# Kernel tuning notes

Measured on AMD Instinct MI355X. Metric: run time of the kernel, lower is better.

## Reference

```python
import jax, jax.numpy as jnp
import numpy as np

H, C = 8, 32          # heads, channels per head; H*C = 256 triggers the LN branch
N_NODES = 30000       # nodes per node type
N_EDGES = 100000      # edges per edge type
N_TYPES = 6           # hardwired edge types (all src = Package_Name)
D_IN = 128            # raw input feature dim (Package_Name stays at 128)
LRELU_SLOPE = 0.2     # PyG GATConv default negative_slope


def _segment_softmax(e, dst, n):
    # softmax of per-edge logits e [E,H] grouped by destination node
    m = jax.ops.segment_max(e, dst, num_segments=n)
    ex = jnp.exp(e - m[dst])
    den = jax.ops.segment_sum(ex, dst, num_segments=n)
    return ex / (den[dst] + 1e-16)


def _gat(x_src, x_tgt, src, dst, Ws, Wd, a_s, a_d, b):
    # bipartite GATConv, concat heads, no self loops, no edge features
    hs = (x_src @ Ws).reshape(-1, H, C)   # [Ns,H,C]
    hd = (x_tgt @ Wd).reshape(-1, H, C)   # [Nt,H,C]
    es = jnp.einsum('nhc,hc->nh', hs, a_s)
    ed = jnp.einsum('nhc,hc->nh', hd, a_d)
    e = jax.nn.leaky_relu(es[src] + ed[dst], negative_slope=LRELU_SLOPE)  # [E,H]
    n = x_tgt.shape[0]
    alpha = _segment_softmax(e, dst, n)                                   # [E,H]
    msg = hs[src] * alpha[:, :, None]                                     # [E,H,C]
    out = jax.ops.segment_sum(msg, dst, num_segments=n).reshape(n, H * C) + b
    return out, alpha


def _ln_relu(x, g, b):
    mu = x.mean(-1, keepdims=True)
    var = ((x - mu) ** 2).mean(-1, keepdims=True)
    return jax.nn.relu((x - mu) / jnp.sqrt(var + 1e-5) * g + b)


def setup_inputs() -> dict:
    key = jax.random.key(0)
    ks = jax.random.split(key, 16)
    s = 0.05
    return {
        'x_pkg': jax.random.normal(ks[0], (N_NODES, D_IN), jnp.float32),
        'x_tgt': jax.random.normal(ks[1], (N_TYPES, N_NODES, D_IN), jnp.float32),
        'edge_index': jax.random.randint(ks[2], (N_TYPES, 2, N_EDGES), 0, N_NODES, jnp.int32),
        'W1_src': jax.random.normal(ks[3], (N_TYPES, D_IN, H * C), jnp.float32) * s,
        'W1_dst': jax.random.normal(ks[4], (N_TYPES, D_IN, H * C), jnp.float32) * s,
        'att1_src': jax.random.normal(ks[5], (N_TYPES, H, C), jnp.float32) * s,
        'att1_dst': jax.random.normal(ks[6], (N_TYPES, H, C), jnp.float32) * s,
        'b1': jnp.zeros((N_TYPES, H * C), jnp.float32),
        'W2_src': jax.random.normal(ks[7], (N_TYPES, D_IN, H * C), jnp.float32) * s,
        'W2_dst': jax.random.normal(ks[8], (N_TYPES, H * C, H * C), jnp.float32) * s,
        'att2_src': jax.random.normal(ks[9], (N_TYPES, H, C), jnp.float32) * s,
        'att2_dst': jax.random.normal(ks[10], (N_TYPES, H, C), jnp.float32) * s,
        'b2': jnp.zeros((N_TYPES, H * C), jnp.float32),
        'gamma': jnp.ones((N_TYPES, H * C), jnp.float32),
        'beta': jnp.zeros((N_TYPES, H * C), jnp.float32),
        'Wc': jax.random.normal(ks[11], (N_TYPES * H * C + D_IN, 1), jnp.float32) * s,
        'bc': jnp.zeros((1,), jnp.float32),
    }


def reference(x_pkg, x_tgt, edge_index, W1_src, W1_dst, att1_src, att1_dst, b1,
              W2_src, W2_dst, att2_src, att2_dst, b2, gamma, beta, Wc, bc):
    def layer(xt, ei, Ws, Wd, a_s, a_d, bb):
        return _gat(x_pkg, xt, ei[0], ei[1], Ws, Wd, a_s, a_d, bb)

    vlayer = jax.vmap(layer, in_axes=(0, 0, 0, 0, 0, 0, 0))

    # layer 1: Package_Name -> each of 6 target types; Package_Name itself unchanged
    out1, _ = vlayer(x_tgt, edge_index, W1_src, W1_dst, att1_src, att1_dst, b1)
    x1 = jax.vmap(_ln_relu)(out1, gamma, beta)   # module reuses ln1 after both layers

    # layer 2: src features are still the raw 128-d Package_Name features
    out2, alpha2 = vlayer(x1, edge_index, W2_src, W2_dst, att2_src, att2_dst, b2)
    x2 = jax.vmap(_ln_relu)(out2, gamma, beta)

    # global mean pool per node type, concat (6 targets then Package_Name), classify
    pooled = jnp.concatenate([x2.mean(axis=1).reshape(-1), x_pkg.mean(axis=0)])
    logits = pooled @ Wc[:, 0] + bc[0]
    return logits, alpha2
```

## Files before the change

kernel.cpp:

```cpp
#include <hip/hip_runtime.h>
#include <hip/hip_bf16.h>
#include <cstddef>

#define N_NODES 30000
#define N_EDGES 100000
#define N_TYPES 6
#define D_IN 128
#define HC 256
#define NH 8
#define CH 32

typedef __attribute__((ext_vector_type(8))) unsigned short ushort8_t;
typedef __attribute__((ext_vector_type(4))) unsigned short ushort4_t;
typedef __attribute__((ext_vector_type(8))) __bf16 bf16x8;
typedef __attribute__((ext_vector_type(4))) float floatx4;

#define FG_GRID (N_NODES / 4)

__device__ inline unsigned short f2bf(float f) {
    unsigned u = __float_as_uint(f);
    u += 0x7fffu + ((u >> 16) & 1u);
    return (unsigned short)(u >> 16);
}
__device__ inline float bf2f(unsigned short u) {
    return __uint_as_float(((unsigned)u) << 16);
}

__global__ void zero4(float4* __restrict__ p, int n4) {
    int g = blockIdx.x * blockDim.x + threadIdx.x;
    if (g < n4) p[g] = make_float4(0.f, 0.f, 0.f, 0.f);
}
__global__ void zero_i(int* __restrict__ p, int n) {
    int g = blockIdx.x * blockDim.x + threadIdx.x;
    if (g < n) p[g] = 0;
}
__global__ void to_bf16(const float* __restrict__ x, unsigned short* __restrict__ o, int n4) {
    int g = blockIdx.x * blockDim.x + threadIdx.x;
    if (g >= n4) return;
    float4 v = ((const float4*)x)[g];
    ushort4_t p;
    p[0] = f2bf(v.x); p[1] = f2bf(v.y); p[2] = f2bf(v.z); p[3] = f2bf(v.w);
    *(ushort4_t*)&o[(size_t)g * 4] = p;
}

__global__ void hist_all(const int* __restrict__ ei, int* __restrict__ counts) {
    int t = blockIdx.y;
    int e = blockIdx.x * 256 + threadIdx.x;
    if (e < N_EDGES)
        atomicAdd(&counts[t * N_NODES + ei[(size_t)t * 2 * N_EDGES + N_EDGES + e]], 1);
}

#define SCAN_T 1024
#define SCAN_C 30
__global__ __launch_bounds__(1024) void scan_all(const int* __restrict__ counts_g,
                                                 int* __restrict__ row_ptr_g,
                                                 int* __restrict__ cursor_g) {
    int t = blockIdx.x;
    const int* counts = counts_g + t * N_NODES;
    int* row_ptr = row_ptr_g + t * (N_NODES + 1);
    int* cursor = cursor_g + t * N_NODES;
    __shared__ int part[SCAN_T];
    int tid = threadIdx.x;
    int base = tid * SCAN_C;
    int loc[SCAN_C];
    int s = 0;
    #pragma unroll
    for (int i = 0; i < SCAN_C; ++i) {
        int idx = base + i;
        int v = (idx < N_NODES) ? counts[idx] : 0;
        loc[i] = s; s += v;
    }
    part[tid] = s;
    __syncthreads();
    int tot = s;
    for (int d = 1; d < SCAN_T; d <<= 1) {
        int v = (tid >= d) ? part[tid - d] : 0;
        __syncthreads();
        part[tid] += v;
        __syncthreads();
    }
    int off = part[tid] - tot;
    #pragma unroll
    for (int i = 0; i < SCAN_C; ++i) {
        int idx = base + i;
        if (idx < N_NODES) { int r = off + loc[i]; row_ptr[idx] = r; cursor[idx] = r; }
    }
    if (tid == SCAN_T - 1) row_ptr[N_NODES] = part[SCAN_T - 1];
}

__global__ void fill_all(const int* __restrict__ ei, const int* __restrict__ row_ptr_g,
                         int* __restrict__ cursor,
                         int* __restrict__ elist, int* __restrict__ edense) {
    int t = blockIdx.y;
    int e = blockIdx.x * 256 + threadIdx.x;
    if (e < N_EDGES) {
        const int* src = ei + (size_t)t * 2 * N_EDGES;
        const int* dst = src + N_EDGES;
        const int d = dst[e];
        int pos = atomicAdd(&cursor[t * N_NODES + d], 1);
        elist[t * N_EDGES + pos] = src[e];
        int loc = pos - row_ptr_g[t * (N_NODES + 1) + d];
        if (loc < 4)
            edense[((size_t)t * N_NODES + d) * 4 + loc] = src[e];
    }
}

__global__ void att_weight_all(const float* __restrict__ W1d, const float* __restrict__ a1d,
                               const float* __restrict__ W2d, const float* __restrict__ a2d,
                               float* __restrict__ wd1, float* __restrict__ wd2) {
    int g = blockIdx.x * blockDim.x + threadIdx.x;
    const int per_t = (D_IN + HC) * NH;
    if (g >= N_TYPES * per_t) return;
    int t = g / per_t, r = g % per_t;
    if (r < D_IN * NH) {
        int k = r >> 3, h = r & 7;
        const float* wr = W1d + (size_t)t * D_IN * HC + (size_t)k * HC + h * CH;
        const float* ar = a1d + t * HC + h * CH;
        float s = 0.f;
        #pragma unroll
        for (int c = 0; c < CH; ++c) s += wr[c] * ar[c];
        wd1[t * D_IN * NH + h * D_IN + k] = s;
    } else {
        r -= D_IN * NH;
        int k = r >> 3, h = r & 7;
        const float* wr = W2d + (size_t)t * HC * HC + (size_t)k * HC + h * CH;
        const float* ar = a2d + t * HC + h * CH;
        float s = 0.f;
        #pragma unroll
        for (int c = 0; c < CH; ++c) s += wr[c] * ar[c];
        wd2[t * HC * NH + h * HC + k] = s;
    }
}

__global__ __launch_bounds__(256) void wt_prep(const float* __restrict__ W1s,
                                               const float* __restrict__ W2s,
                                               unsigned short* __restrict__ Wt) {
    const int j = blockIdx.z;
    const float* W = (j < 6) ? W1s + (size_t)j * D_IN * HC
                             : W2s + (size_t)(j - 6) * D_IN * HC;
    const int n0 = blockIdx.x * 64;
    const int k0 = blockIdx.y * 32;
    __shared__ unsigned short tile[32][71];
    const int t = threadIdx.x;
    {
        const int k = t >> 3, n = (t & 7) * 8;
        const float4 a = *(const float4*)&W[(size_t)(k0 + k) * HC + n0 + n];
        const float4 b = *(const float4*)&W[(size_t)(k0 + k) * HC + n0 + n + 4];
        tile[k][n + 0] = f2bf(a.x); tile[k][n + 1] = f2bf(a.y);
        tile[k][n + 2] = f2bf(a.z); tile[k][n + 3] = f2bf(a.w);
        tile[k][n + 4] = f2bf(b.x); tile[k][n + 5] = f2bf(b.y);
        tile[k][n + 6] = f2bf(b.z); tile[k][n + 7] = f2bf(b.w);
    }
    __syncthreads();
    {
        const int n = t >> 2, k = (t & 3) * 8;
        ushort8_t v;
        #pragma unroll
        for (int q = 0; q < 8; ++q) v[q] = tile[k + q][n];
        *(ushort8_t*)&Wt[((size_t)j * HC + n0 + n) * D_IN + k0 + k] = v;
    }
}

__global__ __launch_bounds__(256) void ed1_all(const float* __restrict__ x_tgt,
                                               const float* __restrict__ wd1,
                                               float* __restrict__ ed1g) {
    const int t = blockIdx.y;
    const int lane = threadIdx.x & 63;
    const int wv = threadIdx.x >> 6;
    const int n8 = lane >> 3, h = lane & 7;
    const int node = blockIdx.x * 32 + wv * 8 + n8;
    if (node >= N_NODES) return;
    const float* xr = x_tgt + ((size_t)t * N_NODES + node) * D_IN;
    const float* wp = wd1 + t * D_IN * NH + h * D_IN;
    float acc = 0.f;
    #pragma unroll
    for (int k = 0; k < D_IN; k += 4) {
        const float4 x4 = *(const float4*)&xr[k];
        const float4 w4 = *(const float4*)&wp[k];
        acc += x4.x * w4.x + x4.y * w4.y + x4.z * w4.z + x4.w * w4.w;
    }
    ed1g[((size_t)t * N_NODES + node) * NH + h] = acc;
}

__global__ __launch_bounds__(256) void gemm_all(const unsigned short* __restrict__ A,
                                                const unsigned short* __restrict__ Wt,
                                                const float* __restrict__ att1,
                                                const float* __restrict__ att2,
                                                unsigned short* __restrict__ hs_all,
                                                float* __restrict__ es_all) {
    const int j = blockIdx.z;
    const unsigned short* B = Wt + (size_t)j * HC * D_IN;
    const float* att = (j < 6) ? att1 + j * HC : att2 + (j - 6) * HC;
    unsigned short* Cp = hs_all + (size_t)j * N_NODES * HC;
    float* e_out = es_all + (size_t)j * N_NODES * NH;

    __shared__ __align__(16) unsigned short As[64 * 136];
    __shared__ __align__(16) unsigned short Bs[128 * 136];

    const int tid = threadIdx.x;
    const int w = tid >> 6;
    const int lane = tid & 63;
    const int col = lane & 15;
    const int quad = lane >> 4;
    const int m0 = blockIdx.x * 64;
    const int n0 = blockIdx.y * 128;

    {
        const int r = tid >> 2;
        const int kc = (tid & 3) * 8;
        const int gm = m0 + r;
        #pragma unroll
        for (int c = 0; c < 4; ++c) {
            ushort8_t v = (ushort8_t){0, 0, 0, 0, 0, 0, 0, 0};
            if (gm < N_NODES) v = *(const ushort8_t*)&A[(size_t)gm * D_IN + kc + c * 32];
            *(ushort8_t*)&As[r * 136 + kc + c * 32] = v;
        }
    }
    {
        const int r = tid >> 1;
        const int ks = (tid & 1) * 64;
        const unsigned short* br = &B[(size_t)(n0 + r) * D_IN + ks];
        #pragma unroll
        for (int q = 0; q < 8; ++q) {
            ushort8_t v = *(const ushort8_t*)&br[q * 8];
            *(ushort8_t*)&Bs[r * 136 + ks + q * 8] = v;
        }
    }
    __syncthreads();

    floatx4 acc[8];
    #pragma unroll
    for (int ct = 0; ct < 8; ++ct) acc[ct] = (floatx4){0.f, 0.f, 0.f, 0.f};

    #pragma unroll
    for (int ks = 0; ks < 4; ++ks) {
        ushort8_t araw = *(const ushort8_t*)&As[(w * 16 + col) * 136 + ks * 32 + quad * 8];
        bf16x8 af = __builtin_bit_cast(bf16x8, araw);
        #pragma unroll
        for (int ct = 0; ct < 8; ++ct) {
            ushort8_t braw = *(const ushort8_t*)&Bs[(ct * 16 + col) * 136 + ks * 32 + quad * 8];
            bf16x8 bf = __builtin_bit_cast(bf16x8, braw);
            acc[ct] = __builtin_amdgcn_mfma_f32_16x16x32_bf16(af, bf, acc[ct], 0, 0, 0);
        }
    }

    float attv[8];
    #pragma unroll
    for (int ct = 0; ct < 8; ++ct) attv[ct] = att[n0 + ct * 16 + col];
    const int hbase = n0 >> 5;
    #pragma unroll
    for (int r = 0; r < 4; ++r) {
        float h0v = acc[0][r] * attv[0] + acc[1][r] * attv[1];
        float h1v = acc[2][r] * attv[2] + acc[3][r] * attv[3];
        float h2v = acc[4][r] * attv[4] + acc[5][r] * attv[5];
        float h3v = acc[6][r] * attv[6] + acc[7][r] * attv[7];
        #pragma unroll
        for (int off = 1; off < 16; off <<= 1) {
            h0v += __shfl_xor(h0v, off);
            h1v += __shfl_xor(h1v, off);
            h2v += __shfl_xor(h2v, off);
            h3v += __shfl_xor(h3v, off);
        }
        if (col == 0) {
            int gm = m0 + w * 16 + quad * 4 + r;
            if (gm < N_NODES)
                *(float4*)&e_out[gm * NH + hbase] = make_float4(h0v, h1v, h2v, h3v);
        }
    }

    __syncthreads();
    unsigned short* Cs = (unsigned short*)Bs;
    #pragma unroll
    for (int ct = 0; ct < 8; ++ct) {
        const int cc = ct * 16 + col;
        #pragma unroll
        for (int r = 0; r < 4; ++r)
            Cs[(w * 16 + quad * 4 + r) * 144 + cc] = f2bf(acc[ct][r]);
    }
    __syncthreads();
    {
        const int r = tid >> 2;
        const int c0 = (tid & 3) * 32;
        const int gm = m0 + r;
        if (gm < N_NODES) {
            #pragma unroll
            for (int q = 0; q < 4; ++q) {
                ushort8_t v = *(const ushort8_t*)&Cs[r * 144 + c0 + q * 8];
                *(ushort8_t*)&Cp[(size_t)gm * HC + n0 + c0 + q * 8] = v;
            }
        }
    }
}

__device__ inline void edge4(const float* __restrict__ es,
                             const unsigned short* __restrict__ hs,
                             int s_pre, int i, int cm,
                             int h_l, int lane, float ed_mine,
                             float& den, float4& acc) {
    const int i1 = (i + 1 < cm) ? i + 1 : cm;
    const int i2 = (i + 2 < cm) ? i + 2 : cm;
    const int i3 = (i + 3 < cm) ? i + 3 : cm;
    const int s0 = __shfl(s_pre, i);
    const int s1 = __shfl(s_pre, i1);
    const int s2 = __shfl(s_pre, i2);
    const int s3 = __shfl(s_pre, i3);
    float q0 = es[s0 * NH + h_l];
    float q1 = es[s1 * NH + h_l];
    float q2 = es[s2 * NH + h_l];
    float q3 = es[s3 * NH + h_l];
    const ushort4_t v0 = *(const ushort4_t*)&hs[(size_t)s0 * HC + lane * 4];
    const ushort4_t v1 = *(const ushort4_t*)&hs[(size_t)s1 * HC + lane * 4];
    const ushort4_t v2 = *(const ushort4_t*)&hs[(size_t)s2 * HC + lane * 4];
    const ushort4_t v3 = *(const ushort4_t*)&hs[(size_t)s3 * HC + lane * 4];
    q0 += ed_mine; q0 = (q0 >= 0.f) ? q0 : 0.2f * q0;
    q1 += ed_mine; q1 = (q1 >= 0.f) ? q1 : 0.2f * q1;
    q2 += ed_mine; q2 = (q2 >= 0.f) ? q2 : 0.2f * q2;
    q3 += ed_mine; q3 = (q3 >= 0.f) ? q3 : 0.2f * q3;
    const float x0 = __expf(q0);
    const float x1 = (i + 1 <= cm) ? __expf(q1) : 0.f;
    const float x2 = (i + 2 <= cm) ? __expf(q2) : 0.f;
    const float x3 = (i + 3 <= cm) ? __expf(q3) : 0.f;
    den += (x0 + x1) + (x2 + x3);
    acc.x += x0 * bf2f(v0[0]) + x1 * bf2f(v1[0]) + x2 * bf2f(v2[0]) + x3 * bf2f(v3[0]);
    acc.y += x0 * bf2f(v0[1]) + x1 * bf2f(v1[1]) + x2 * bf2f(v2[1]) + x3 * bf2f(v3[1]);
    acc.z += x0 * bf2f(v0[2]) + x1 * bf2f(v1[2]) + x2 * bf2f(v2[2]) + x3 * bf2f(v3[2]);
    acc.w += x0 * bf2f(v0[3]) + x1 * bf2f(v1[3]) + x2 * bf2f(v2[3]) + x3 * bf2f(v3[3]);
}

__device__ inline void edge1(const float* __restrict__ es,
                             const unsigned short* __restrict__ hs,
                             int s, int h_l, int lane, float ed_mine,
                             float& den, float4& acc) {
    float x = es[s * NH + h_l] + ed_mine;
    x = (x >= 0.f) ? x : 0.2f * x;
    const float ex = __expf(x);
    den += ex;
    const ushort4_t hv = *(const ushort4_t*)&hs[(size_t)s * HC + lane * 4];
    acc.x += ex * bf2f(hv[0]); acc.y += ex * bf2f(hv[1]);
    acc.z += ex * bf2f(hv[2]); acc.w += ex * bf2f(hv[3]);
}

__global__ __launch_bounds__(256) void fused_gather_all(
        const int* __restrict__ row_ptr_g, const int* __restrict__ elist_g,
        const int* __restrict__ edense_g,
        const float* __restrict__ es_all, const float* __restrict__ ed1g,
        const unsigned short* __restrict__ hs_all,
        const float* __restrict__ b1, const float* __restrict__ b2,
        const float* __restrict__ gamma, const float* __restrict__ beta,
        const float* __restrict__ wd2,
        float* __restrict__ ed2g_all, float* __restrict__ deng_all,
        float* __restrict__ ppart) {
    const int t = blockIdx.y;
    const int* row_ptr = row_ptr_g + t * (N_NODES + 1);
    const int* elist = elist_g + t * N_EDGES;
    const int* eden = edense_g + (size_t)t * N_NODES * 4;
    const float* es1 = es_all + (size_t)t * N_NODES * NH;
    const float* es2 = es_all + (size_t)(6 + t) * N_NODES * NH;
    const unsigned short* hs1 = hs_all + (size_t)t * N_NODES * HC;
    const unsigned short* hs2 = hs_all + (size_t)(6 + t) * N_NODES * HC;
    const float* gam = gamma + t * HC;
    const float* bet = beta + t * HC;
    const float* w2 = wd2 + t * HC * NH;
    float* ed2g = ed2g_all + (size_t)t * N_NODES * NH;
    float* deng = deng_all + (size_t)t * N_NODES * NH;

    const int lane = threadIdx.x & 63;
    const int w = threadIdx.x >> 6;
    const int d = blockIdx.x * 4 + w;
    const int h_l = lane >> 3;

    const float ed_mine = ed1g[((size_t)t * N_NODES + d) * NH + h_l];
    int dw = 0;
    if (lane < 4) dw = eden[d * 4 + lane];
    const int e0 = row_ptr[d], e1n = row_ptr[d + 1];
    const int cnt = e1n - e0;
    const bool fast = (cnt > 0) && (cnt <= 4);

    int s_pre = 0;
    if (!fast) {
        if (lane < cnt) s_pre = elist[e0 + lane];
    }

    float den1 = 0.f, den2 = 0.f;
    float4 acc1 = make_float4(0.f, 0.f, 0.f, 0.f);
    float4 acc2 = make_float4(0.f, 0.f, 0.f, 0.f);

    float q20, q21, q22, q23;
    ushort4_t v20, v21, v22, v23;

    if (fast) {
        const int s0 = __shfl(dw, 0);
        const int s1 = __shfl(dw, 1);
        const int s2 = __shfl(dw, 2);
        const int s3 = __shfl(dw, 3);
        float q10 = es1[s0 * NH + h_l];
        float q11 = es1[s1 * NH + h_l];
        float q12 = es1[s2 * NH + h_l];
        float q13 = es1[s3 * NH + h_l];
        const ushort4_t v10 = *(const ushort4_t*)&hs1[(size_t)s0 * HC + lane * 4];
        const ushort4_t v11 = *(const ushort4_t*)&hs1[(size_t)s1 * HC + lane * 4];
        const ushort4_t v12 = *(const ushort4_t*)&hs1[(size_t)s2 * HC + lane * 4];
        const ushort4_t v13 = *(const ushort4_t*)&hs1[(size_t)s3 * HC + lane * 4];
        q20 = es2[s0 * NH + h_l];
        q21 = es2[s1 * NH + h_l];
        q22 = es2[s2 * NH + h_l];
        q23 = es2[s3 * NH + h_l];
        v20 = *(const ushort4_t*)&hs2[(size_t)s0 * HC + lane * 4];
        v21 = *(const ushort4_t*)&hs2[(size_t)s1 * HC + lane * 4];
        v22 = *(const ushort4_t*)&hs2[(size_t)s2 * HC + lane * 4];
        v23 = *(const ushort4_t*)&hs2[(size_t)s3 * HC + lane * 4];
        q10 += ed_mine; q10 = (q10 >= 0.f) ? q10 : 0.2f * q10;
        q11 += ed_mine; q11 = (q11 >= 0.f) ? q11 : 0.2f * q11;
        q12 += ed_mine; q12 = (q12 >= 0.f) ? q12 : 0.2f * q12;
        q13 += ed_mine; q13 = (q13 >= 0.f) ? q13 : 0.2f * q13;
        const float x0 = __expf(q10);
        const float x1 = (cnt > 1) ? __expf(q11) : 0.f;
        const float x2 = (cnt > 2) ? __expf(q12) : 0.f;
        const float x3 = (cnt > 3) ? __expf(q13) : 0.f;
        den1 = (x0 + x1) + (x2 + x3);
        acc1.x = x0 * bf2f(v10[0]) + x1 * bf2f(v11[0]) + x2 * bf2f(v12[0]) + x3 * bf2f(v13[0]);
        acc1.y = x0 * bf2f(v10[1]) + x1 * bf2f(v11[1]) + x2 * bf2f(v12[1]) + x3 * bf2f(v13[1]);
        acc1.z = x0 * bf2f(v10[2]) + x1 * bf2f(v11[2]) + x2 * bf2f(v12[2]) + x3 * bf2f(v13[2]);
        acc1.w = x0 * bf2f(v10[3]) + x1 * bf2f(v11[3]) + x2 * bf2f(v12[3]) + x3 * bf2f(v13[3]);
    } else if (cnt > 0) {
        const int c1 = (cnt < 64) ? cnt : 64;
        const int cm = c1 - 1;
        for (int i = 0; i < c1; i += 4)
            edge4(es1, hs1, s_pre, i, cm, h_l, lane, ed_mine, den1, acc1);
        if (cnt > 64)
            for (int ii = e0 + 64; ii < e1n; ++ii)
                edge1(es1, hs1, elist[ii], h_l, lane, ed_mine, den1, acc1);
    }

    const float inv1 = 1.f / (den1 + 1e-16f);
    const float4 bv1 = *(const float4*)&b1[t * HC + lane * 4];
    acc1.x = acc1.x * inv1 + bv1.x; acc1.y = acc1.y * inv1 + bv1.y;
    acc1.z = acc1.z * inv1 + bv1.z; acc1.w = acc1.w * inv1 + bv1.w;

    float s1 = acc1.x + acc1.y + acc1.z + acc1.w;
    float s2 = acc1.x * acc1.x + acc1.y * acc1.y + acc1.z * acc1.z + acc1.w * acc1.w;
    #pragma unroll
    for (int off = 1; off < 64; off <<= 1) { s1 += __shfl_xor(s1, off); s2 += __shfl_xor(s2, off); }
    const float mu = s1 * (1.f / 256.f);
    const float var = s2 * (1.f / 256.f) - mu * mu;
    const float rstd = rsqrtf(var + 1e-5f);
    const float4 g4 = *(const float4*)&gam[lane * 4];
    const float4 b4 = *(const float4*)&bet[lane * 4];
    const float ya0 = fmaxf((acc1.x - mu) * rstd * g4.x + b4.x, 0.f);
    const float ya1 = fmaxf((acc1.y - mu) * rstd * g4.y + b4.y, 0.f);
    const float ya2 = fmaxf((acc1.z - mu) * rstd * g4.z + b4.z, 0.f);
    const float ya3 = fmaxf((acc1.w - mu) * rstd * g4.w + b4.w, 0.f);

    __shared__ __align__(16) float ya_s[4][256];
    {
        const int c0 = lane * 4;
        const int widx = (c0 & ~31) | ((c0 & 31) ^ ((lane >> 3) << 2));
        *(float4*)&ya_s[w][widx] = make_float4(ya0, ya1, ya2, ya3);
    }
    const int k8 = lane >> 3;
    const int hh = lane & 7;
    const float* w2h = w2 + hh * HC;
    float e2 = 0.f;
    #pragma unroll
    for (int jj = 0; jj < 8; ++jj) {
        const int idx = k8 * 32 + ((jj * 4) ^ (k8 << 2));
        const float4 y = *(const float4*)&ya_s[w][idx];
        const float4 wv = *(const float4*)&w2h[k8 * 32 + jj * 4];
        e2 += y.x * wv.x + y.y * wv.y + y.z * wv.z + y.w * wv.w;
    }
    e2 += __shfl_xor(e2, 8);
    e2 += __shfl_xor(e2, 16);
    e2 += __shfl_xor(e2, 32);
    if (lane < 8) ed2g[d * NH + lane] = e2;
    const float ed2_mine = __shfl(e2, h_l);

    if (fast) {
        q20 += ed2_mine; q20 = (q20 >= 0.f) ? q20 : 0.2f * q20;
        q21 += ed2_mine; q21 = (q21 >= 0.f) ? q21 : 0.2f * q21;
        q22 += ed2_mine; q22 = (q22 >= 0.f) ? q22 : 0.2f * q22;
        q23 += ed2_mine; q23 = (q23 >= 0.f) ? q23 : 0.2f * q23;
        const float x0 = __expf(q20);
        const float x1 = (cnt > 1) ? __expf(q21) : 0.f;
        const float x2 = (cnt > 2) ? __expf(q22) : 0.f;
        const float x3 = (cnt > 3) ? __expf(q23) : 0.f;
        den2 = (x0 + x1) + (x2 + x3);
        acc2.x = x0 * bf2f(v20[0]) + x1 * bf2f(v21[0]) + x2 * bf2f(v22[0]) + x3 * bf2f(v23[0]);
        acc2.y = x0 * bf2f(v20[1]) + x1 * bf2f(v21[1]) + x2 * bf2f(v22[1]) + x3 * bf2f(v23[1]);
        acc2.z = x0 * bf2f(v20[2]) + x1 * bf2f(v21[2]) + x2 * bf2f(v22[2]) + x3 * bf2f(v23[2]);
        acc2.w = x0 * bf2f(v20[3]) + x1 * bf2f(v21[3]) + x2 * bf2f(v22[3]) + x3 * bf2f(v23[3]);
    } else if (cnt > 0) {
        const int c1 = (cnt < 64) ? cnt : 64;
        const int cm = c1 - 1;
        for (int i = 0; i < c1; i += 4)
            edge4(es2, hs2, s_pre, i, cm, h_l, lane, ed2_mine, den2, acc2);
        if (cnt > 64)
            for (int ii = e0 + 64; ii < e1n; ++ii)
                edge1(es2, hs2, elist[ii], h_l, lane, ed2_mine, den2, acc2);
    }

    if ((lane & 7) == 0) deng[d * NH + h_l] = den2;
    const float inv2 = 1.f / (den2 + 1e-16f);
    const float4 bv2 = *(const float4*)&b2[t * HC + lane * 4];
    acc2.x = acc2.x * inv2 + bv2.x; acc2.y = acc2.y * inv2 + bv2.y;
    acc2.z = acc2.z * inv2 + bv2.z; acc2.w = acc2.w * inv2 + bv2.w;

    float t1 = acc2.x + acc2.y + acc2.z + acc2.w;
    float t2 = acc2.x * acc2.x + acc2.y * acc2.y + acc2.z * acc2.z + acc2.w * acc2.w;
    #pragma unroll
    for (int off = 1; off < 64; off <<= 1) { t1 += __shfl_xor(t1, off); t2 += __shfl_xor(t2, off); }
    const float mu2 = t1 * (1.f / 256.f);
    const float var2 = t2 * (1.f / 256.f) - mu2 * mu2;
    const float rstd2 = rsqrtf(var2 + 1e-5f);
    float4 pool;
    pool.x = fmaxf((acc2.x - mu2) * rstd2 * g4.x + b4.x, 0.f);
    pool.y = fmaxf((acc2.y - mu2) * rstd2 * g4.y + b4.y, 0.f);
    pool.z = fmaxf((acc2.z - mu2) * rstd2 * g4.z + b4.z, 0.f);
    pool.w = fmaxf((acc2.w - mu2) * rstd2 * g4.w + b4.w, 0.f);

    __shared__ __align__(16) float sacc[4][260];
    *(float4*)&sacc[w][lane * 4] = pool;
    __syncthreads();
    const int tid = threadIdx.x;
    float tot = sacc[0][tid] + sacc[1][tid] + sacc[2][tid] + sacc[3][tid];
    ppart[((size_t)t * FG_GRID + blockIdx.x) * HC + tid] = tot;
}

__global__ __launch_bounds__(256) void pool_reduce_all(const float* __restrict__ ppart,
                                                       float* __restrict__ psums) {
    int t = blockIdx.y;
    const float* part = ppart + (size_t)t * FG_GRID * HC;
    int tid = threadIdx.x;
    float acc = 0.f;
    for (int b = blockIdx.x; b < FG_GRID; b += gridDim.x)
        acc += part[(size_t)b * HC + tid];
    atomicAdd(&psums[t * HC + tid], acc);
}

__global__ __launch_bounds__(256) void alpha_all(const int* __restrict__ ei,
                          const float* __restrict__ es_all,
                          const float* __restrict__ ed2g_all,
                          const float* __restrict__ deng_all,
                          float* __restrict__ out) {
    int t = blockIdx.y;
    int e = blockIdx.x * 256 + threadIdx.x;
    if (e >= N_EDGES) return;
    const int* src = ei + (size_t)t * 2 * N_EDGES;
    const int* dst = src + N_EDGES;
    const int s = src[e], d = dst[e];
    const float* esp = es_all + (size_t)(6 + t) * N_NODES * NH + (size_t)s * NH;
    const float* edp = ed2g_all + (size_t)t * N_NODES * NH + (size_t)d * NH;
    const float* dnp = deng_all + (size_t)t * N_NODES * NH + (size_t)d * NH;
    const float4 ea = *(const float4*)esp;
    const float4 eb = *(const float4*)(esp + 4);
    const float4 da = *(const float4*)edp;
    const float4 db = *(const float4*)(edp + 4);
    const float4 na = *(const float4*)dnp;
    const float4 nb = *(const float4*)(dnp + 4);
    float x[8];
    x[0] = ea.x + da.x; x[1] = ea.y + da.y; x[2] = ea.z + da.z; x[3] = ea.w + da.w;
    x[4] = eb.x + db.x; x[5] = eb.y + db.y; x[6] = eb.z + db.z; x[7] = eb.w + db.w;
    float n[8] = {na.x, na.y, na.z, na.w, nb.x, nb.y, nb.z, nb.w};
    float* op = out + (size_t)t * N_EDGES * NH + (size_t)e * NH;
    #pragma unroll
    for (int h = 0; h < 8; ++h) {
        float v = x[h];
        v = (v >= 0.f) ? v : 0.2f * v;
        op[h] = __expf(v) / (n[h] + 1e-16f);
    }
}

__global__ __launch_bounds__(256) void pkg_accum(const float* __restrict__ x, float* __restrict__ sums) {
    int tid = threadIdx.x;
    int col = tid & 127;
    int rof = tid >> 7;
    float acc = 0.f;
    for (int r = blockIdx.x * 2 + rof; r < N_NODES; r += gridDim.x * 2)
        acc += x[(size_t)r * D_IN + col];
    atomicAdd(&sums[col], acc);
}

__global__ __launch_bounds__(256) void logits_k(const float* __restrict__ psums,
                                                const float* __restrict__ ksums,
                                                const float* __restrict__ Wc,
                                                const float* __restrict__ bc,
                                                float* __restrict__ out) {
    int tid = threadIdx.x;
    const float inv = 1.f / (float)N_NODES;
    float acc = 0.f;
    for (int i = tid; i < N_TYPES * HC; i += 256) acc += psums[i] * inv * Wc[i];
    if (tid < D_IN) acc += ksums[tid] * inv * Wc[N_TYPES * HC + tid];
    #pragma unroll
    for (int off = 32; off; off >>= 1) acc += __shfl_down(acc, off);
    __shared__ float w[4];
    if ((tid & 63) == 0) w[tid >> 6] = acc;
    __syncthreads();
    if (tid == 0) out[0] = w[0] + w[1] + w[2] + w[3] + bc[0];
}

static inline void zf(float* p, int n, hipStream_t stream) {
    int n4 = (n + 3) >> 2;
    zero4<<<(n4 + 255) / 256, 256, 0, stream>>>((float4*)p, n4);
}

extern "C" void kernel_launch(void* const* d_in, const int* in_sizes, int n_in,
                              void* d_out, int out_size, void* d_ws, size_t ws_size,
                              hipStream_t stream) {
    const float* x_pkg    = (const float*)d_in[0];
    const float* x_tgt    = (const float*)d_in[1];
    const int*   ei       = (const int*)d_in[2];
    const float* W1_src   = (const float*)d_in[3];
    const float* W1_dst   = (const float*)d_in[4];
    const float* att1_src = (const float*)d_in[5];
    const float* att1_dst = (const float*)d_in[6];
    const float* b1       = (const float*)d_in[7];
    const float* W2_src   = (const float*)d_in[8];
    const float* W2_dst   = (const float*)d_in[9];
    const float* att2_src = (const float*)d_in[10];
    const float* att2_dst = (const float*)d_in[11];
    const float* b2       = (const float*)d_in[12];
    const float* gamma    = (const float*)d_in[13];
    const float* beta     = (const float*)d_in[14];
    const float* Wc       = (const float*)d_in[15];
    const float* bc       = (const float*)d_in[16];
    float* out = (float*)d_out;

    char* wsb = (char*)d_ws;
    unsigned short* xpkg_bf = (unsigned short*)wsb;
    unsigned short* hs_all  = xpkg_bf + (size_t)N_NODES * D_IN;
    float* es_all   = (float*)(hs_all + (size_t)12 * N_NODES * HC);
    float* ed2g_all = es_all + (size_t)12 * N_NODES * NH;
    float* deng_all = ed2g_all + (size_t)N_TYPES * N_NODES * NH;
    float* psums    = deng_all + (size_t)N_TYPES * N_NODES * NH;
    float* ksums    = psums + N_TYPES * HC;
    float* wd1      = ksums + D_IN;
    float* wd2      = wd1 + N_TYPES * D_IN * NH;
    unsigned short* Wt = (unsigned short*)(wd2 + N_TYPES * HC * NH);
    float* ed1g     = (float*)(Wt + (size_t)12 * HC * D_IN);
    float* ppart    = ed1g + (size_t)N_TYPES * N_NODES * NH;
    int* counts  = (int*)(ppart + (size_t)N_TYPES * FG_GRID * HC);
    int* row_ptr = counts + N_TYPES * N_NODES;
    int* cursor  = row_ptr + N_TYPES * (N_NODES + 1);
    int* elist   = cursor + N_TYPES * N_NODES;
    int* edense  = elist + N_TYPES * N_EDGES;

    dim3 egrid((N_EDGES + 255) / 256, N_TYPES);

    zf(psums, N_TYPES * HC + D_IN, stream);
    pkg_accum<<<256, 256, 0, stream>>>(x_pkg, ksums);
    {
        int tot = N_TYPES * (D_IN + HC) * NH;
        att_weight_all<<<(tot + 255) / 256, 256, 0, stream>>>(W1_dst, att1_dst, W2_dst, att2_dst, wd1, wd2);
    }
    {
        dim3 g(4, 4, 12);
        wt_prep<<<g, 256, 0, stream>>>(W1_src, W2_src, Wt);
    }
    {
        dim3 g((N_NODES + 31) / 32, N_TYPES);
        ed1_all<<<g, 256, 0, stream>>>(x_tgt, wd1, ed1g);
    }
    to_bf16<<<((N_NODES * D_IN / 4) + 255) / 256, 256, 0, stream>>>(x_pkg, xpkg_bf, N_NODES * D_IN / 4);
    zero_i<<<(N_TYPES * N_NODES + 255) / 256, 256, 0, stream>>>(counts, N_TYPES * N_NODES);
    zero_i<<<(N_TYPES * N_NODES * 4 + 255) / 256, 256, 0, stream>>>(edense, N_TYPES * N_NODES * 4);
    hist_all<<<egrid, 256, 0, stream>>>(ei, counts);
    scan_all<<<N_TYPES, SCAN_T, 0, stream>>>(counts, row_ptr, cursor);
    fill_all<<<egrid, 256, 0, stream>>>(ei, row_ptr, cursor, elist, edense);

    {
        dim3 g((N_NODES + 63) / 64, 2, 12);
        gemm_all<<<g, 256, 0, stream>>>(xpkg_bf, Wt, att1_src, att2_src,
                                        hs_all, es_all);
    }

    {
        dim3 g(FG_GRID, N_TYPES);
        fused_gather_all<<<g, 256, 0, stream>>>(row_ptr, elist, edense, es_all, ed1g, hs_all,
                                                b1, b2, gamma, beta, wd2,
                                                ed2g_all, deng_all, ppart);
    }
    {
        dim3 g(64, N_TYPES);
        pool_reduce_all<<<g, 256, 0, stream>>>(ppart, psums);
    }
    {
        dim3 g((N_EDGES + 255) / 256, N_TYPES);
        alpha_all<<<g, 256, 0, stream>>>(ei, es_all, ed2g_all, deng_all, out + 1);
    }

    logits_k<<<1, 256, 0, stream>>>(psums, ksums, Wc, bc, out);
}
```

Baseline: 848.5 us.

## Process two destination nodes per wavefront with batched fast-path gathers

Each wavefront in the fused gather kernel now handles two destination nodes instead of one, halving the grid. Both nodes' fast-path gathers (attention logits and bf16 features for both layers) are issued up front, so more memory loads are in flight per wave and per-type constants are loaded once. The cost is higher register pressure from holding two FastBuf sets, which may lower occupancy. The shared ya buffer is reused by both nodes in sequence within the same wave.

Measured after the change: 794.2 us. 1.07x faster.

```diff
diff --git a/kernel.cpp b/kernel.cpp
--- a/kernel.cpp
+++ b/kernel.cpp
@@ -15,7 +15,7 @@
 typedef __attribute__((ext_vector_type(8))) __bf16 bf16x8;
 typedef __attribute__((ext_vector_type(4))) float floatx4;
 
-#define FG_GRID (N_NODES / 4)
+#define FG_GRID (N_NODES / 8)
 
 __device__ inline unsigned short f2bf(float f) {
     unsigned u = __float_as_uint(f);
@@ -340,6 +340,156 @@
     acc.z += ex * bf2f(hv[2]); acc.w += ex * bf2f(hv[3]);
 }
 
+struct FastBuf {
+    float q10, q11, q12, q13, q20, q21, q22, q23;
+    ushort4_t v10, v11, v12, v13, v20, v21, v22, v23;
+};
+
+__device__ inline FastBuf node_load_fast(int dw, int h_l, int lane,
+        const float* __restrict__ es1, const float* __restrict__ es2,
+        const unsigned short* __restrict__ hs1, const unsigned short* __restrict__ hs2) {
+    FastBuf b;
+    const int s0 = __shfl(dw, 0);
+    const int s1 = __shfl(dw, 1);
+    const int s2 = __shfl(dw, 2);
+    const int s3 = __shfl(dw, 3);
+    b.q10 = es1[s0 * NH + h_l];
+    b.q11 = es1[s1 * NH + h_l];
+    b.q12 = es1[s2 * NH + h_l];
+    b.q13 = es1[s3 * NH + h_l];
+    b.v10 = *(const ushort4_t*)&hs1[(size_t)s0 * HC + lane * 4];
+    b.v11 = *(const ushort4_t*)&hs1[(size_t)s1 * HC + lane * 4];
+    b.v12 = *(const ushort4_t*)&hs1[(size_t)s2 * HC + lane * 4];
+    b.v13 = *(const ushort4_t*)&hs1[(size_t)s3 * HC + lane * 4];
+    b.q20 = es2[s0 * NH + h_l];
+    b.q21 = es2[s1 * NH + h_l];
+    b.q22 = es2[s2 * NH + h_l];
+    b.q23 = es2[s3 * NH + h_l];
+    b.v20 = *(const ushort4_t*)&hs2[(size_t)s0 * HC + lane * 4];
+    b.v21 = *(const ushort4_t*)&hs2[(size_t)s1 * HC + lane * 4];
+    b.v22 = *(const ushort4_t*)&hs2[(size_t)s2 * HC + lane * 4];
+    b.v23 = *(const ushort4_t*)&hs2[(size_t)s3 * HC + lane * 4];
+    return b;
+}
+
+__device__ inline float4 node_math(
+        bool fast, int cnt, int e0, int e1n, int s_pre, float ed_mine,
+        const FastBuf& fb,
+        const float* __restrict__ es1, const float* __restrict__ es2,
+        const unsigned short* __restrict__ hs1, const unsigned short* __restrict__ hs2,
+        const int* __restrict__ elist,
+        const float4& bv1, const float4& bv2, const float4& g4, const float4& b4,
+        float* ya_row, const float* __restrict__ w2h,
+        int lane, int h_l, int d,
+        float* __restrict__ ed2g, float* __restrict__ deng) {
+    float den1 = 0.f, den2 = 0.f;
+    float4 acc1 = make_float4(0.f, 0.f, 0.f, 0.f);
+    float4 acc2 = make_float4(0.f, 0.f, 0.f, 0.f);
+
+    if (fast) {
+        float q10 = fb.q10 + ed_mine; q10 = (q10 >= 0.f) ? q10 : 0.2f * q10;
+        float q11 = fb.q11 + ed_mine; q11 = (q11 >= 0.f) ? q11 : 0.2f * q11;
+        float q12 = fb.q12 + ed_mine; q12 = (q12 >= 0.f) ? q12 : 0.2f * q12;
+        float q13 = fb.q13 + ed_mine; q13 = (q13 >= 0.f) ? q13 : 0.2f * q13;
+        const float x0 = __expf(q10);
+        const float x1 = (cnt > 1) ? __expf(q11) : 0.f;
+        const float x2 = (cnt > 2) ? __expf(q12) : 0.f;
+        const float x3 = (cnt > 3) ? __expf(q13) : 0.f;
+        den1 = (x0 + x1) + (x2 + x3);
+        acc1.x = x0 * bf2f(fb.v10[0]) + x1 * bf2f(fb.v11[0]) + x2 * bf2f(fb.v12[0]) + x3 * bf2f(fb.v13[0]);
+        acc1.y = x0 * bf2f(fb.v10[1]) + x1 * bf2f(fb.v11[1]) + x2 * bf2f(fb.v12[1]) + x3 * bf2f(fb.v13[1]);
+        acc1.z = x0 * bf2f(fb.v10[2]) + x1 * bf2f(fb.v11[2]) + x2 * bf2f(fb.v12[2]) + x3 * bf2f(fb.v13[2]);
+        acc1.w = x0 * bf2f(fb.v10[3]) + x1 * bf2f(fb.v11[3]) + x2 * bf2f(fb.v12[3]) + x3 * bf2f(fb.v13[3]);
+    } else if (cnt > 0) {
+        const int c1 = (cnt < 64) ? cnt : 64;
+        const int cm = c1 - 1;
+        for (int i = 0; i < c1; i += 4)
+            edge4(es1, hs1, s_pre, i, cm, h_l, lane, ed_mine, den1, acc1);
+        if (cnt > 64)
+            for (int ii = e0 + 64; ii < e1n; ++ii)
+                edge1(es1, hs1, elist[ii], h_l, lane, ed_mine, den1, acc1);
+    }
+
+    const float inv1 = 1.f / (den1 + 1e-16f);
+    acc1.x = acc1.x * inv1 + bv1.x; acc1.y = acc1.y * inv1 + bv1.y;
+    acc1.z = acc1.z * inv1 + bv1.z; acc1.w = acc1.w * inv1 + bv1.w;
+
+    float s1 = acc1.x + acc1.y + acc1.z + acc1.w;
+    float s2 = acc1.x * acc1.x + acc1.y * acc1.y + acc1.z * acc1.z + acc1.w * acc1.w;
+    #pragma unroll
+    for (int off = 1; off < 64; off <<= 1) { s1 += __shfl_xor(s1, off); s2 += __shfl_xor(s2, off); }
+    const float mu = s1 * (1.f / 256.f);
+    const float var = s2 * (1.f / 256.f) - mu * mu;
+    const float rstd = rsqrtf(var + 1e-5f);
+    const float ya0 = fmaxf((acc1.x - mu) * rstd * g4.x + b4.x, 0.f);
+    const float ya1 = fmaxf((acc1.y - mu) * rstd * g4.y + b4.y, 0.f);
+    const float ya2 = fmaxf((acc1.z - mu) * rstd * g4.z + b4.z, 0.f);
+    const float ya3 = fmaxf((acc1.w - mu) * rstd * g4.w + b4.w, 0.f);
+
+    {
+        const int c0 = lane * 4;
+        const int widx = (c0 & ~31) | ((c0 & 31) ^ ((lane >> 3) << 2));
+        *(float4*)&ya_row[widx] = make_float4(ya0, ya1, ya2, ya3);
+    }
+    const int k8 = lane >> 3;
+    float e2 = 0.f;
+    #pragma unroll
+    for (int jj = 0; jj < 8; ++jj) {
+        const int idx = k8 * 32 + ((jj * 4) ^ (k8 << 2));
+        const float4 y = *(const float4*)&ya_row[idx];
+        const float4 wv = *(const float4*)&w2h[k8 * 32 + jj * 4];
+        e2 += y.x * wv.x + y.y * wv.y + y.z * wv.z + y.w * wv.w;
+    }
+    e2 += __shfl_xor(e2, 8);
+    e2 += __shfl_xor(e2, 16);
+    e2 += __shfl_xor(e2, 32);
+    if (lane < 8) ed2g[d * NH + lane] = e2;
+    const float ed2_mine = __shfl(e2, h_l);
+
+    if (fast) {
+        float q20 = fb.q20 + ed2_mine; q20 = (q20 >= 0.f) ? q20 : 0.2f * q20;
+        float q21 = fb.q21 + ed2_mine; q21 = (q21 >= 0.f) ? q21 : 0.2f * q21;
+        float q22 = fb.q22 + ed2_mine; q22 = (q22 >= 0.f) ? q22 : 0.2f * q22;
+        float q23 = fb.q23 + ed2_mine; q23 = (q23 >= 0.f) ? q23 : 0.2f * q23;
+        const float x0 = __expf(q20);
+        const float x1 = (cnt > 1) ? __expf(q21) : 0.f;
+        const float x2 = (cnt > 2) ? __expf(q22) : 0.f;
+        const float x3 = (cnt > 3) ? __expf(q23) : 0.f;
+        den2 = (x0 + x1) + (x2 + x3);
+        acc2.x = x0 * bf2f(fb.v20[0]) + x1 * bf2f(fb.v21[0]) + x2 * bf2f(fb.v22[0]) + x3 * bf2f(fb.v23[0]);
+        acc2.y = x0 * bf2f(fb.v20[1]) + x1 * bf2f(fb.v21[1]) + x2 * bf2f(fb.v22[1]) + x3 * bf2f(fb.v23[1]);
+        acc2.z = x0 * bf2f(fb.v20[2]) + x1 * bf2f(fb.v21[2]) + x2 * bf2f(fb.v22[2]) + x3 * bf2f(fb.v23[2]);
+        acc2.w = x0 * bf2f(fb.v20[3]) + x1 * bf2f(fb.v21[3]) + x2 * bf2f(fb.v22[3]) + x3 * bf2f(fb.v23[3]);
+    } else if (cnt > 0) {
+        const int c1 = (cnt < 64) ? cnt : 64;
+        const int cm = c1 - 1;
+        for (int i = 0; i < c1; i += 4)
+            edge4(es2, hs2, s_pre, i, cm, h_l, lane, ed2_mine, den2, acc2);
+        if (cnt > 64)
+            for (int ii = e0 + 64; ii < e1n; ++ii)
+                edge1(es2, hs2, elist[ii], h_l, lane, ed2_mine, den2, acc2);
+    }
+
+    if ((lane & 7) == 0) deng[d * NH + h_l] = den2;
+    const float inv2 = 1.f / (den2 + 1e-16f);
+    acc2.x = acc2.x * inv2 + bv2.x; acc2.y = acc2.y * inv2 + bv2.y;
+    acc2.z = acc2.z * inv2 + bv2.z; acc2.w = acc2.w * inv2 + bv2.w;
+
+    float t1 = acc2.x + acc2.y + acc2.z + acc2.w;
+    float t2 = acc2.x * acc2.x + acc2.y * acc2.y + acc2.z * acc2.z + acc2.w * acc2.w;
+    #pragma unroll
+    for (int off = 1; off < 64; off <<= 1) { t1 += __shfl_xor(t1, off); t2 += __shfl_xor(t2, off); }
+    const float mu2 = t1 * (1.f / 256.f);
+    const float var2 = t2 * (1.f / 256.f) - mu2 * mu2;
+    const float rstd2 = rsqrtf(var2 + 1e-5f);
+    float4 pool;
+    pool.x = fmaxf((acc2.x - mu2) * rstd2 * g4.x + b4.x, 0.f);
+    pool.y = fmaxf((acc2.y - mu2) * rstd2 * g4.y + b4.y, 0.f);
+    pool.z = fmaxf((acc2.z - mu2) * rstd2 * g4.z + b4.z, 0.f);
+    pool.w = fmaxf((acc2.w - mu2) * rstd2 * g4.w + b4.w, 0.f);
+    return pool;
+}
+
 __global__ __launch_bounds__(256) void fused_gather_all(
         const int* __restrict__ row_ptr_g, const int* __restrict__ elist_g,
         const int* __restrict__ edense_g,
@@ -358,164 +508,58 @@
     const float* es2 = es_all + (size_t)(6 + t) * N_NODES * NH;
     const unsigned short* hs1 = hs_all + (size_t)t * N_NODES * HC;
     const unsigned short* hs2 = hs_all + (size_t)(6 + t) * N_NODES * HC;
-    const float* gam = gamma + t * HC;
-    const float* bet = beta + t * HC;
-    const float* w2 = wd2 + t * HC * NH;
     float* ed2g = ed2g_all + (size_t)t * N_NODES * NH;
     float* deng = deng_all + (size_t)t * N_NODES * NH;
 
     const int lane = threadIdx.x & 63;
     const int w = threadIdx.x >> 6;
-    const int d = blockIdx.x * 4 + w;
+    const int dA = blockIdx.x * 8 + w * 2;
+    const int dB = dA + 1;
     const int h_l = lane >> 3;
 
-    const float ed_mine = ed1g[((size_t)t * N_NODES + d) * NH + h_l];
-    int dw = 0;
-    if (lane < 4) dw = eden[d * 4 + lane];
-    const int e0 = row_ptr[d], e1n = row_ptr[d + 1];
-    const int cnt = e1n - e0;
-    const bool fast = (cnt > 0) && (cnt <= 4);
-
-    int s_pre = 0;
-    if (!fast) {
-        if (lane < cnt) s_pre = elist[e0 + lane];
-    }
-
-    float den1 = 0.f, den2 = 0.f;
-    float4 acc1 = make_float4(0.f, 0.f, 0.f, 0.f);
-    float4 acc2 = make_float4(0.f, 0.f, 0.f, 0.f);
-
-    float q20, q21, q22, q23;
-    ushort4_t v20, v21, v22, v23;
-
-    if (fast) {
-        const int s0 = __shfl(dw, 0);
-        const int s1 = __shfl(dw, 1);
-        const int s2 = __shfl(dw, 2);
-        const int s3 = __shfl(dw, 3);
-        float q10 = es1[s0 * NH + h_l];
-        float q11 = es1[s1 * NH + h_l];
-        float q12 = es1[s2 * NH + h_l];
-        float q13 = es1[s3 * NH + h_l];
-        const ushort4_t v10 = *(const ushort4_t*)&hs1[(size_t)s0 * HC + lane * 4];
-        const ushort4_t v11 = *(const ushort4_t*)&hs1[(size_t)s1 * HC + lane * 4];
-        const ushort4_t v12 = *(const ushort4_t*)&hs1[(size_t)s2 * HC + lane * 4];
-        const ushort4_t v13 = *(const ushort4_t*)&hs1[(size_t)s3 * HC + lane * 4];
-        q20 = es2[s0 * NH + h_l];
-        q21 = es2[s1 * NH + h_l];
-        q22 = es2[s2 * NH + h_l];
-        q23 = es2[s3 * NH + h_l];
-        v20 = *(const ushort4_t*)&hs2[(size_t)s0 * HC + lane * 4];
-        v21 = *(const ushort4_t*)&hs2[(size_t)s1 * HC + lane * 4];
-        v22 = *(const ushort4_t*)&hs2[(size_t)s2 * HC + lane * 4];
-        v23 = *(const ushort4_t*)&hs2[(size_t)s3 * HC + lane * 4];
-        q10 += ed_mine; q10 = (q10 >= 0.f) ? q10 : 0.2f * q10;
-        q11 += ed_mine; q11 = (q11 >= 0.f) ? q11 : 0.2f * q11;
-        q12 += ed_mine; q12 = (q12 >= 0.f) ? q12 : 0.2f * q12;
-        q13 += ed_mine; q13 = (q13 >= 0.f) ? q13 : 0.2f * q13;
-        const float x0 = __expf(q10);
-        const float x1 = (cnt > 1) ? __expf(q11) : 0.f;
-        const float x2 = (cnt > 2) ? __expf(q12) : 0.f;
-        const float x3 = (cnt > 3) ? __expf(q13) : 0.f;
-        den1 = (x0 + x1) + (x2 + x3);
-        acc1.x = x0 * bf2f(v10[0]) + x1 * bf2f(v11[0]) + x2 * bf2f(v12[0]) + x3 * bf2f(v13[0]);
-        acc1.y = x0 * bf2f(v10[1]) + x1 * bf2f(v11[1]) + x2 * bf2f(v12[1]) + x3 * bf2f(v13[1]);
-        acc1.z = x0 * bf2f(v10[2]) + x1 * bf2f(v11[2]) + x2 * bf2f(v12[2]) + x3 * bf2f(v13[2]);
-        acc1.w = x0 * bf2f(v10[3]) + x1 * bf2f(v11[3]) + x2 * bf2f(v12[3]) + x3 * bf2f(v13[3]);
-    } else if (cnt > 0) {
-        const int c1 = (cnt < 64) ? cnt : 64;
-        const int cm = c1 - 1;
-        for (int i = 0; i < c1; i += 4)
-            edge4(es1, hs1, s_pre, i, cm, h_l, lane, ed_mine, den1, acc1);
-        if (cnt > 64)
-            for (int ii = e0 + 64; ii < e1n; ++ii)
-                edge1(es1, hs1, elist[ii], h_l, lane, ed_mine, den1, acc1);
-    }
-
-    const float inv1 = 1.f / (den1 + 1e-16f);
+    const float edmA = ed1g[((size_t)t * N_NODES + dA) * NH + h_l];
+    const float edmB = ed1g[((size_t)t * N_NODES + dB) * NH + h_l];
+    int dwA = 0, dwB = 0;
+    if (lane < 4) {
+        dwA = eden[dA * 4 + lane];
+        dwB = eden[dB * 4 + lane];
+    }
+    const int e0A = row_ptr[dA];
+    const int e1nA = row_ptr[dA + 1];
+    const int e1nB = row_ptr[dA + 2];
+    const int e0B = e1nA;
+    const int cntA = e1nA - e0A, cntB = e1nB - e0B;
+    const bool fastA = (cntA > 0) && (cntA <= 4);
+    const bool fastB = (cntB > 0) && (cntB <= 4);
+
+    int s_preA = 0, s_preB = 0;
+    if (!fastA) { if (lane < cntA) s_preA = elist[e0A + lane]; }
+    if (!fastB) { if (lane < cntB) s_preB = elist[e0B + lane]; }
+
+    FastBuf fbA, fbB;
+    if (fastA) fbA = node_load_fast(dwA, h_l, lane, es1, es2, hs1, hs2);
+    if (fastB) fbB = node_load_fast(dwB, h_l, lane, es1, es2, hs1, hs2);
+
     const float4 bv1 = *(const float4*)&b1[t * HC + lane * 4];
-    acc1.x = acc1.x * inv1 + bv1.x; acc1.y = acc1.y * inv1 + bv1.y;
-    acc1.z = acc1.z * inv1 + bv1.z; acc1.w = acc1.w * inv1 + bv1.w;
-
-    float s1 = acc1.x + acc1.y + acc1.z + acc1.w;
-    float s2 = acc1.x * acc1.x + acc1.y * acc1.y + acc1.z * acc1.z + acc1.w * acc1.w;
-    #pragma unroll
-    for (int off = 1; off < 64; off <<= 1) { s1 += __shfl_xor(s1, off); s2 += __shfl_xor(s2, off); }
-    const float mu = s1 * (1.f / 256.f);
-    const float var = s2 * (1.f / 256.f) - mu * mu;
-    const float rstd = rsqrtf(var + 1e-5f);
-    const float4 g4 = *(const float4*)&gam[lane * 4];
-    const float4 b4 = *(const float4*)&bet[lane * 4];
-    const float ya0 = fmaxf((acc1.x - mu) * rstd * g4.x + b4.x, 0.f);
-    const float ya1 = fmaxf((acc1.y - mu) * rstd * g4.y + b4.y, 0.f);
-    const float ya2 = fmaxf((acc1.z - mu) * rstd * g4.z + b4.z, 0.f);
-    const float ya3 = fmaxf((acc1.w - mu) * rstd * g4.w + b4.w, 0.f);
+    const float4 bv2 = *(const float4*)&b2[t * HC + lane * 4];
+    const float4 g4 = *(const float4*)&gamma[t * HC + lane * 4];
+    const float4 b4 = *(const float4*)&beta[t * HC + lane * 4];
+    const float* w2h = wd2 + t * HC * NH + (lane & 7) * HC;
 
     __shared__ __align__(16) float ya_s[4][256];
-    {
-        const int c0 = lane * 4;
-        const int widx = (c0 & ~31) | ((c0 & 31) ^ ((lane >> 3) << 2));
-        *(float4*)&ya_s[w][widx] = make_float4(ya0, ya1, ya2, ya3);
-    }
-    const int k8 = lane >> 3;
-    const int hh = lane & 7;
-    const float* w2h = w2 + hh * HC;
-    float e2 = 0.f;
-    #pragma unroll
-    for (int jj = 0; jj < 8; ++jj) {
-        const int idx = k8 * 32 + ((jj * 4) ^ (k8 << 2));
-        const float4 y = *(const float4*)&ya_s[w][idx];
-        const float4 wv = *(const float4*)&w2h[k8 * 32 + jj * 4];
-        e2 += y.x * wv.x + y.y * wv.y + y.z * wv.z + y.w * wv.w;
-    }
-    e2 += __shfl_xor(e2, 8);
-    e2 += __shfl_xor(e2, 16);
-    e2 += __shfl_xor(e2, 32);
-    if (lane < 8) ed2g[d * NH + lane] = e2;
-    const float ed2_mine = __shfl(e2, h_l);
-
-    if (fast) {
-        q20 += ed2_mine; q20 = (q20 >= 0.f) ? q20 : 0.2f * q20;
-        q21 += ed2_mine; q21 = (q21 >= 0.f) ? q21 : 0.2f * q21;
-        q22 += ed2_mine; q22 = (q22 >= 0.f) ? q22 : 0.2f * q22;
-        q23 += ed2_mine; q23 = (q23 >= 0.f) ? q23 : 0.2f * q23;
-        const float x0 = __expf(q20);
-        const float x1 = (cnt > 1) ? __expf(q21) : 0.f;
-        const float x2 = (cnt > 2) ? __expf(q22) : 0.f;
-        const float x3 = (cnt > 3) ? __expf(q23) : 0.f;
-        den2 = (x0 + x1) + (x2 + x3);
-        acc2.x = x0 * bf2f(v20[0]) + x1 * bf2f(v21[0]) + x2 * bf2f(v22[0]) + x3 * bf2f(v23[0]);
-        acc2.y = x0 * bf2f(v20[1]) + x1 * bf2f(v21[1]) + x2 * bf2f(v22[1]) + x3 * bf2f(v23[1]);
-        acc2.z = x0 * bf2f(v20[2]) + x1 * bf2f(v21[2]) + x2 * bf2f(v22[2]) + x3 * bf2f(v23[2]);
-        acc2.w = x0 * bf2f(v20[3]) + x1 * bf2f(v21[3]) + x2 * bf2f(v22[3]) + x3 * bf2f(v23[3]);
-    } else if (cnt > 0) {
-        const int c1 = (cnt < 64) ? cnt : 64;
-        const int cm = c1 - 1;
-        for (int i = 0; i < c1; i += 4)
-            edge4(es2, hs2, s_pre, i, cm, h_l, lane, ed2_mine, den2, acc2);
-        if (cnt > 64)
-            for (int ii = e0 + 64; ii < e1n; ++ii)
-                edge1(es2, hs2, elist[ii], h_l, lane, ed2_mine, den2, acc2);
-    }
-
-    if ((lane & 7) == 0) deng[d * NH + h_l] = den2;
-    const float inv2 = 1.f / (den2 + 1e-16f);
-    const float4 bv2 = *(const float4*)&b2[t * HC + lane * 4];
-    acc2.x = acc2.x * inv2 + bv2.x; acc2.y = acc2.y * inv2 + bv2.y;
-    acc2.z = acc2.z * inv2 + bv2.z; acc2.w = acc2.w * inv2 + bv2.w;
-
-    float t1 = acc2.x + acc2.y + acc2.z + acc2.w;
-    float t2 = acc2.x * acc2.x + acc2.y * acc2.y + acc2.z * acc2.z + acc2.w * acc2.w;
-    #pragma unroll
-    for (int off = 1; off < 64; off <<= 1) { t1 += __shfl_xor(t1, off); t2 += __shfl_xor(t2, off); }
-    const float mu2 = t1 * (1.f / 256.f);
-    const float var2 = t2 * (1.f / 256.f) - mu2 * mu2;
-    const float rstd2 = rsqrtf(var2 + 1e-5f);
+
+    const float4 poolA = node_math(fastA, cntA, e0A, e1nA, s_preA, edmA, fbA,
+                                   es1, es2, hs1, hs2, elist, bv1, bv2, g4, b4,
+                                   &ya_s[w][0], w2h, lane, h_l, dA, ed2g, deng);
+    const float4 poolB = node_math(fastB, cntB, e0B, e1nB, s_preB, edmB, fbB,
+                                   es1, es2, hs1, hs2, elist, bv1, bv2, g4, b4,
+                                   &ya_s[w][0], w2h, lane, h_l, dB, ed2g, deng);
+
     float4 pool;
-    pool.x = fmaxf((acc2.x - mu2) * rstd2 * g4.x + b4.x, 0.f);
-    pool.y = fmaxf((acc2.y - mu2) * rstd2 * g4.y + b4.y, 0.f);
-    pool.z = fmaxf((acc2.z - mu2) * rstd2 * g4.z + b4.z, 0.f);
-    pool.w = fmaxf((acc2.w - mu2) * rstd2 * g4.w + b4.w, 0.f);
+    pool.x = poolA.x + poolB.x;
+    pool.y = poolA.y + poolB.y;
+    pool.z = poolA.z + poolB.z;
+    pool.w = poolA.w + poolB.w;
 
     __shared__ __align__(16) float sacc[4][260];
     *(float4*)&sacc[w][lane * 4] = pool;
```
